# Performance work log

Hardware: AMD Instinct MI355X
Metric: run time of the kernel (lower is better)

Reference implementation:

```python
import jax, jax.numpy as jnp
import numpy as np

N = 100000      # nodes
E = 1600000     # edges (avg degree 16)
NFEAT = 16
HID = 64
OUT = 4
K = 3           # TAGConv hops
L = 4           # number of TAGConv layers


def setup_inputs() -> dict:
    key = jax.random.key(0)
    ks = jax.random.split(key, 6)
    x = jax.random.normal(ks[0], (N, NFEAT), dtype=jnp.float32)
    edge_index = jax.random.randint(ks[1], (2, E), 0, N, dtype=jnp.int64)
    # TAGConv has one (bias-free) linear per hop k=0..K, plus a per-layer bias.
    W0 = jax.random.normal(ks[2], (K + 1, NFEAT, HID), dtype=jnp.float32) * 0.1
    b0 = jnp.zeros((HID,), dtype=jnp.float32)
    Wh = jax.random.normal(ks[3], (L - 1, K + 1, HID, HID), dtype=jnp.float32) * 0.1
    bh = jnp.zeros((L - 1, HID), dtype=jnp.float32)
    fcW = jax.random.normal(ks[4], (HID, OUT), dtype=jnp.float32) * 0.1
    fcb = jnp.zeros((OUT,), dtype=jnp.float32)
    return dict(x=x, edge_index=edge_index, W0=W0, b0=b0, Wh=Wh, bh=bh, fcW=fcW, fcb=fcb)


def _gcn_norm(src, dst, num_nodes):
    # symmetric GCN normalization, no self-loops (PyG TAGConv default)
    ones = jnp.ones(src.shape, dtype=jnp.float32)
    deg = jax.ops.segment_sum(ones, dst, num_segments=num_nodes)
    dinv = jnp.where(deg > 0, 1.0 / jnp.sqrt(jnp.maximum(deg, 1e-12)), 0.0)
    return dinv[src] * dinv[dst]  # [E]


def _tag_conv(x, src, dst, norm, W, b):
    # out = sum_{k=0..K} (A_norm^k x) W_k + b
    out = x @ W[0]
    h = x
    for k in range(1, W.shape[0]):
        h = jax.ops.segment_sum(norm[:, None] * h[src], dst, num_segments=x.shape[0])
        out = out + h @ W[k]
    return out + b


def reference(x, edge_index, W0, b0, Wh, bh, fcW, fcb):
    src, dst = edge_index[0], edge_index[1]
    norm = _gcn_norm(src, dst, x.shape[0])
    h = jax.nn.relu(_tag_conv(x, src, dst, norm, W0, b0))  # conv0 (+relu, dropout=identity)
    for l in range(Wh.shape[0] - 1):  # middle convs with relu
        h = jax.nn.relu(_tag_conv(h, src, dst, norm, Wh[l], bh[l]))
    h = _tag_conv(h, src, dst, norm, Wh[-1], bh[-1])  # last conv, no relu
    return h @ fcW + fcb  # [N, OUT]
```

## Files before the change

kernel.cpp:

```cpp
#include <hip/hip_runtime.h>
#include <hip/hip_fp16.h>

constexpr int Nn   = 100000;
constexpr int Ne   = 1600000;
constexpr int NF   = 16;
constexpr int HID  = 64;
constexpr int NOUT = 4;

constexpr int NBUK  = 391;
constexpr int CHUNK = 2048;
constexpr int NB1   = (Ne + CHUNK - 1) / CHUNK;
constexpr int NS    = NBUK * NB1;
constexpr int STASH = 6144;

union H8 { float4 f4; __half h[8]; };
union H4 { float2 f2; __half h[4]; };


__global__ __launch_bounds__(256) void bhist_kernel(const int* __restrict__ dst,
                                                    int* __restrict__ ghist) {
    __shared__ int h[NBUK];
    int t = threadIdx.x;
    int b = blockIdx.x;
    for (int i = t; i < NBUK; i += 256) h[i] = 0;
    __syncthreads();
    int e0 = b * CHUNK;
    int e1 = (e0 + CHUNK < Ne) ? e0 + CHUNK : Ne;
    for (int e = e0 + t; e < e1; e += 256) atomicAdd(&h[dst[e] >> 8], 1);
    __syncthreads();
    for (int i = t; i < NBUK; i += 256) ghist[i * NB1 + b] = h[i];
}

__global__ __launch_bounds__(256) void scan1g_kernel(int* __restrict__ g,
                                                     int* __restrict__ bsum) {
    __shared__ int lds[256];
    int t = threadIdx.x;
    int base = blockIdx.x * 1024 + t * 4;
    int v0 = (base + 0 < NS) ? g[base + 0] : 0;
    int v1 = (base + 1 < NS) ? g[base + 1] : 0;
    int v2 = (base + 2 < NS) ? g[base + 2] : 0;
    int v3 = (base + 3 < NS) ? g[base + 3] : 0;
    lds[t] = v0 + v1 + v2 + v3;
    __syncthreads();
    for (int off = 1; off < 256; off <<= 1) {
        int a = lds[t];
        int b = (t >= off) ? lds[t - off] : 0;
        __syncthreads();
        lds[t] = a + b;
        __syncthreads();
    }
    int excl = (t > 0) ? lds[t - 1] : 0;
    if (base + 0 < NS) g[base + 0] = excl;
    if (base + 1 < NS) g[base + 1] = excl + v0;
    if (base + 2 < NS) g[base + 2] = excl + v0 + v1;
    if (base + 3 < NS) g[base + 3] = excl + v0 + v1 + v2;
    if (t == 255) bsum[blockIdx.x] = lds[255];
}

__global__ __launch_bounds__(512) void scan2g_kernel(int* __restrict__ bsum, int nb) {
    __shared__ int lds[512];
    int t = threadIdx.x;
    int v = (t < nb) ? bsum[t] : 0;
    lds[t] = v;
    __syncthreads();
    for (int off = 1; off < 512; off <<= 1) {
        int a = lds[t];
        int b = (t >= off) ? lds[t - off] : 0;
        __syncthreads();
        lds[t] = a + b;
        __syncthreads();
    }
    if (t < nb) bsum[t] = lds[t] - v;
}

__global__ __launch_bounds__(256) void scan3g_kernel(int* __restrict__ g,
                                                     const int* __restrict__ bsum) {
    int i = blockIdx.x * 256 + threadIdx.x;
    if (i < NS) g[i] += bsum[i >> 10];
}

__global__ __launch_bounds__(256) void bscatter_kernel(const int* __restrict__ src,
                                                       const int* __restrict__ dst,
                                                       const int* __restrict__ ghist,
                                                       int2* __restrict__ tmp) {
    __shared__ int hb[NBUK];
    __shared__ int cur[NBUK];
    int t = threadIdx.x;
    int b = blockIdx.x;
    for (int i = t; i < NBUK; i += 256) {
        hb[i] = ghist[i * NB1 + b];
        cur[i] = 0;
    }
    __syncthreads();
    int e0 = b * CHUNK;
    int e1 = (e0 + CHUNK < Ne) ? e0 + CHUNK : Ne;
    for (int e = e0 + t; e < e1; e += 256) {
        int d = dst[e];
        int s = src[e];
        int bin = d >> 8;
        int r = atomicAdd(&cur[bin], 1);
        tmp[hb[bin] + r] = make_int2(s, d);
    }
}

__global__ __launch_bounds__(256) void bcsr_kernel(const int2* __restrict__ tmp,
                                                   const int* __restrict__ ghist,
                                                   int* __restrict__ rowptr,
                                                   float* __restrict__ dinv,
                                                   int* __restrict__ colsrc) {
    __shared__ int2 stash[STASH];
    __shared__ int h[256];
    __shared__ int hs[256];
    __shared__ int cur[256];
    int t = threadIdx.x;
    int b = blockIdx.x;
    int lo = ghist[b * NB1];
    int hi = (b < NBUK - 1) ? ghist[(b + 1) * NB1] : Ne;
    int sz = hi - lo;
    h[t] = 0;
    cur[t] = 0;
    __syncthreads();
    for (int i = t; i < sz; i += 256) {
        int2 rec = tmp[lo + i];
        if (i < STASH) stash[i] = rec;
        atomicAdd(&h[rec.y & 255], 1);
    }
    __syncthreads();
    int myh = h[t];
    hs[t] = myh;
    __syncthreads();
    for (int off = 1; off < 256; off <<= 1) {
        int a = hs[t];
        int bb = (t >= off) ? hs[t - off] : 0;
        __syncthreads();
        hs[t] = a + bb;
        __syncthreads();
    }
    int excl = hs[t] - myh;
    __syncthreads();
    hs[t] = excl;
    int d = (b << 8) + t;
    if (d < Nn) {
        rowptr[d] = lo + excl;
        dinv[d] = (myh > 0) ? rsqrtf((float)myh) : 0.0f;
    }
    if (b == NBUK - 1 && t == 0) rowptr[Nn] = Ne;
    __syncthreads();
    for (int i = t; i < sz; i += 256) {
        int2 rec = (i < STASH) ? stash[i] : tmp[lo + i];
        int bin = rec.y & 255;
        int r = atomicAdd(&cur[bin], 1);
        colsrc[lo + hs[bin] + r] = rec.x;
    }
}

__global__ __launch_bounds__(256) void fill_kernel(const int* __restrict__ colsrc,
                                                   const float* __restrict__ dinv,
                                                   int2* __restrict__ edge2) {
    int e = blockIdx.x * 256 + threadIdx.x;
    if (e < Ne) {
        int s = colsrc[e];
        edge2[e] = make_int2(s, __float_as_int(dinv[s]));
    }
}

__global__ __launch_bounds__(256) void xcvt_kernel(const float* __restrict__ x,
                                                   __half* __restrict__ xh) {
    int i = blockIdx.x * 256 + threadIdx.x;
    if (i < Nn * NF / 4) {
        float4 v = reinterpret_cast<const float4*>(x)[i];
        H4 o;
        o.h[0] = __float2half(v.x);
        o.h[1] = __float2half(v.y);
        o.h[2] = __float2half(v.z);
        o.h[3] = __float2half(v.w);
        reinterpret_cast<float2*>(xh)[i] = o.f2;
    }
}


__global__ __launch_bounds__(256) void pull64h_kernel(const __half* __restrict__ hin,
                                                      const int* __restrict__ rowptr,
                                                      const int2* __restrict__ edge2,
                                                      const float* __restrict__ dinv,
                                                      __half* __restrict__ hout) {
    int lane = threadIdx.x & 63;
    int q  = lane & 3;
    int eo = (lane >> 2) & 3;
    int g  = lane >> 4;
    int n = blockIdx.x * 16 + (threadIdx.x >> 6) * 4 + g;
    if (n >= Nn) return;
    int r0 = rowptr[n];
    int r1 = rowptr[n + 1];
    float a[16];
#pragma unroll
    for (int j = 0; j < 16; ++j) a[j] = 0.f;
#pragma unroll 2
    for (int e = r0 + eo; e < r1; e += 4) {
        int2 ed = edge2[e];
        float w = __int_as_float(ed.y);
        const float4* rp = reinterpret_cast<const float4*>(hin + (size_t)ed.x * 64 + q * 16);
        H8 u0, u1;
        u0.f4 = rp[0];
        u1.f4 = rp[1];
#pragma unroll
        for (int j = 0; j < 8; ++j) a[j] += w * __half2float(u0.h[j]);
#pragma unroll
        for (int j = 0; j < 8; ++j) a[8 + j] += w * __half2float(u1.h[j]);
    }
#pragma unroll
    for (int off = 4; off <= 8; off <<= 1)
#pragma unroll
        for (int j = 0; j < 16; ++j) a[j] += __shfl_xor(a[j], off);
    if (eo == 0) {
        float dn = dinv[n];
        H8 o0, o1;
#pragma unroll
        for (int j = 0; j < 8; ++j) o0.h[j] = __float2half(a[j] * dn);
#pragma unroll
        for (int j = 0; j < 8; ++j) o1.h[j] = __float2half(a[8 + j] * dn);
        float4* op = reinterpret_cast<float4*>(hout + (size_t)n * 64 + q * 16);
        op[0] = o0.f4;
        op[1] = o1.f4;
    }
}

__global__ __launch_bounds__(256) void pull16h_kernel(const __half* __restrict__ hin,
                                                      const int* __restrict__ rowptr,
                                                      const int2* __restrict__ edge2,
                                                      const float* __restrict__ dinv,
                                                      __half* __restrict__ hout) {
    int lane = threadIdx.x & 63;
    int q  = lane & 1;
    int eo = (lane >> 1) & 3;
    int g  = lane >> 3;
    int n = blockIdx.x * 32 + (threadIdx.x >> 6) * 8 + g;
    if (n >= Nn) return;
    int r0 = rowptr[n];
    int r1 = rowptr[n + 1];
    float a[8];
#pragma unroll
    for (int j = 0; j < 8; ++j) a[j] = 0.f;
#pragma unroll 2
    for (int e = r0 + eo; e < r1; e += 4) {
        int2 ed = edge2[e];
        float w = __int_as_float(ed.y);
        H8 u;
        u.f4 = *reinterpret_cast<const float4*>(hin + (size_t)ed.x * 16 + q * 8);
#pragma unroll
        for (int j = 0; j < 8; ++j) a[j] += w * __half2float(u.h[j]);
    }
#pragma unroll
    for (int off = 2; off <= 4; off <<= 1)
#pragma unroll
        for (int j = 0; j < 8; ++j) a[j] += __shfl_xor(a[j], off);
    if (eo == 0) {
        float dn = dinv[n];
        H8 o;
#pragma unroll
        for (int j = 0; j < 8; ++j) o.h[j] = __float2half(a[j] * dn);
        *reinterpret_cast<float4*>(hout + (size_t)n * 16 + q * 8) = o.f4;
    }
}

template <int ADDBIAS>
__global__ __launch_bounds__(256) void pull4_kernel(const float* __restrict__ uin,
                                                    const float* __restrict__ gadd,
                                                    const int* __restrict__ rowptr,
                                                    const int2* __restrict__ edge2,
                                                    const float* __restrict__ dinv,
                                                    const float* __restrict__ beff,
                                                    float* __restrict__ out) {
    int lane = threadIdx.x & 63;
    int eo = lane & 15;
    int n = blockIdx.x * 16 + ((threadIdx.x >> 6) << 2) + (lane >> 4);
    if (n >= Nn) return;
    int r0 = rowptr[n];
    int r1 = rowptr[n + 1];
    float ax = 0.f, ay = 0.f, az = 0.f, aw = 0.f;
    for (int e = r0 + eo; e < r1; e += 16) {
        int2 ed = edge2[e];
        float w = __int_as_float(ed.y);
        float4 v = *reinterpret_cast<const float4*>(uin + (size_t)ed.x * 4);
        ax += w * v.x;
        ay += w * v.y;
        az += w * v.z;
        aw += w * v.w;
    }
#pragma unroll
    for (int off = 1; off < 16; off <<= 1) {
        ax += __shfl_xor(ax, off);
        ay += __shfl_xor(ay, off);
        az += __shfl_xor(az, off);
        aw += __shfl_xor(aw, off);
    }
    if (eo == 0) {
        float dn = dinv[n];
        float4 g = *reinterpret_cast<const float4*>(gadd + (size_t)n * 4);
        float4 o;
        o.x = g.x + dn * ax;
        o.y = g.y + dn * ay;
        o.z = g.z + dn * az;
        o.w = g.w + dn * aw;
        if (ADDBIAS) {
            o.x += beff[0]; o.y += beff[1]; o.z += beff[2]; o.w += beff[3];
        }
        *reinterpret_cast<float4*>(out + (size_t)n * 4) = o;
    }
}


template <int KS>
__global__ __launch_bounds__(256) void gemm4_kernel(const __half* __restrict__ S0,
                                                    const __half* __restrict__ S1,
                                                    const __half* __restrict__ S2,
                                                    const __half* __restrict__ S3,
                                                    const float* __restrict__ W,
                                                    const float* __restrict__ bias,
                                                    __half* __restrict__ out) {
    constexpr int PITCH = KS + 4;
    __shared__ float Ht[128 * PITCH];
    __shared__ float Wt[KS * 64];
    int t = threadIdx.x;
    int c4 = t & 15;
    int r8 = t >> 4;
    int r0 = blockIdx.x * 128;
    float acc[8][4];
#pragma unroll
    for (int j = 0; j < 8; ++j)
#pragma unroll
        for (int d = 0; d < 4; ++d) acc[j][d] = 0.f;

    const __half* Ss[4] = {S0, S1, S2, S3};
#pragma unroll
    for (int k = 0; k < 4; ++k) {
        const __half* S = Ss[k];
        for (int i = t; i < KS * 16; i += 256)
            *reinterpret_cast<float4*>(&Wt[i * 4]) =
                *reinterpret_cast<const float4*>(W + (size_t)k * KS * 64 + i * 4);
        for (int i = t; i < 128 * (KS / 8); i += 256) {
            int r = i / (KS / 8);
            int c8 = i % (KS / 8);
            int row = r0 + r;
            float* hp = &Ht[r * PITCH + c8 * 8];
            if (row < Nn) {
                H8 u;
                u.f4 = *reinterpret_cast<const float4*>(S + (size_t)row * KS + c8 * 8);
#pragma unroll
                for (int j = 0; j < 8; ++j) hp[j] = __half2float(u.h[j]);
            } else {
#pragma unroll
                for (int j = 0; j < 8; ++j) hp[j] = 0.f;
            }
        }
        __syncthreads();
#pragma unroll 4
        for (int f = 0; f < KS; ++f) {
            float4 b4 = *reinterpret_cast<const float4*>(&Wt[f * 64 + c4 * 4]);
#pragma unroll
            for (int j = 0; j < 8; ++j) {
                float a = Ht[(r8 + 16 * j) * PITCH + f];
                acc[j][0] += a * b4.x;
                acc[j][1] += a * b4.y;
                acc[j][2] += a * b4.z;
                acc[j][3] += a * b4.w;
            }
        }
        __syncthreads();
    }
    float4 bi = *reinterpret_cast<const float4*>(bias + c4 * 4);
#pragma unroll
    for (int j = 0; j < 8; ++j) {
        int row = r0 + r8 + 16 * j;
        if (row < Nn) {
            H4 o;
            o.h[0] = __float2half(fmaxf(acc[j][0] + bi.x, 0.f));
            o.h[1] = __float2half(fmaxf(acc[j][1] + bi.y, 0.f));
            o.h[2] = __float2half(fmaxf(acc[j][2] + bi.z, 0.f));
            o.h[3] = __float2half(fmaxf(acc[j][3] + bi.w, 0.f));
            *reinterpret_cast<float2*>(out + (size_t)row * 64 + c4 * 4) = o.f2;
        }
    }
}

__global__ __launch_bounds__(256) void weff_kernel(const float* __restrict__ W,
                                                   const float* __restrict__ b,
                                                   const float* __restrict__ fcW,
                                                   const float* __restrict__ fcb,
                                                   float* __restrict__ Wg,
                                                   float* __restrict__ beff) {
    int t = threadIdx.x;
    int k = t >> 6, c = t & 63;
    const float* wrow = W + (size_t)t * 64;
    float a0 = 0.f, a1 = 0.f, a2 = 0.f, a3 = 0.f;
    for (int d = 0; d < 64; ++d) {
        float w = wrow[d];
        a0 += w * fcW[d * 4 + 0];
        a1 += w * fcW[d * 4 + 1];
        a2 += w * fcW[d * 4 + 2];
        a3 += w * fcW[d * 4 + 3];
    }
    float4 o; o.x = a0; o.y = a1; o.z = a2; o.w = a3;
    *reinterpret_cast<float4*>(Wg + k * 256 + c * 4) = o;
    if (t < 4) {
        float s = fcb[t];
        for (int d = 0; d < 64; ++d) s += b[d] * fcW[d * 4 + t];
        beff[t] = s;
    }
}

__global__ __launch_bounds__(256) void gemmG_kernel(const __half* __restrict__ h,
                                                    const float* __restrict__ Wg,
                                                    float* __restrict__ G) {
    __shared__ float Ht[64 * 65];
    __shared__ float Wl[1024];
    int t = threadIdx.x;
    int r0 = blockIdx.x * 64;
    for (int i = t; i < 256; i += 256)
        *reinterpret_cast<float4*>(&Wl[i * 4]) = *reinterpret_cast<const float4*>(Wg + i * 4);
    for (int i = t; i < 64 * 8; i += 256) {
        int r = i >> 3;
        int c8 = i & 7;
        int row = r0 + r;
        float* hp = &Ht[r * 65 + c8 * 8];
        if (row < Nn) {
            H8 u;
            u.f4 = *reinterpret_cast<const float4*>(h + (size_t)row * 64 + c8 * 8);
#pragma unroll
            for (int j = 0; j < 8; ++j) hp[j] = __half2float(u.h[j]);
        } else {
#pragma unroll
            for (int j = 0; j < 8; ++j) hp[j] = 0.f;
        }
    }
    __syncthreads();
    int r = t & 63;
    int k = t >> 6;
    float a0 = 0.f, a1 = 0.f, a2 = 0.f, a3 = 0.f;
#pragma unroll 8
    for (int c = 0; c < 64; ++c) {
        float hv = Ht[r * 65 + c];
        const float* wp = &Wl[k * 256 + c * 4];
        a0 += hv * wp[0];
        a1 += hv * wp[1];
        a2 += hv * wp[2];
        a3 += hv * wp[3];
    }
    int row = r0 + r;
    if (row < Nn) {
        float4 o; o.x = a0; o.y = a1; o.z = a2; o.w = a3;
        *reinterpret_cast<float4*>(G + (size_t)k * Nn * 4 + (size_t)row * 4) = o;
    }
}


extern "C" void kernel_launch(void* const* d_in, const int* in_sizes, int n_in,
                              void* d_out, int out_size, void* d_ws, size_t ws_size,
                              hipStream_t stream) {
    const float* x   = (const float*)d_in[0];
    const int*   ei  = (const int*)d_in[1];
    const float* W0  = (const float*)d_in[2];
    const float* b0  = (const float*)d_in[3];
    const float* Wh  = (const float*)d_in[4];
    const float* bh  = (const float*)d_in[5];
    const float* fcW = (const float*)d_in[6];
    const float* fcb = (const float*)d_in[7];
    float* out = (float*)d_out;

    const int* src = ei;
    const int* dst = ei + Ne;

    int*    rowptr = (int*)d_ws;
    int2*   edge2  = (int2*)(rowptr + 100004);
    int*    ghist  = (int*)(rowptr + 100004 + 2 * Ne);
    int*    bsum   = ghist + 305792;
    float*  dinv   = (float*)(bsum + 512);
    float*  Wg     = dinv + Nn;
    float*  beff   = Wg + 1024;
    __half* xh     = (__half*)(beff + 16);
    __half* H0     = xh + (size_t)Nn * NF;
    __half* H1     = H0 + (size_t)Nn * HID;
    __half* H2     = H1 + (size_t)Nn * HID;
    __half* H3     = H2 + (size_t)Nn * HID;
    float*  G      = (float*)(H3 + (size_t)Nn * HID);
    float*  G0     = G + 0 * (size_t)Nn * 4;
    float*  G1     = G + 1 * (size_t)Nn * 4;
    float*  G2     = G + 2 * (size_t)Nn * 4;
    float*  G3     = G + 3 * (size_t)Nn * 4;
    float*  T      = G + 4 * (size_t)Nn * 4;
    float*  T2     = G + 5 * (size_t)Nn * 4;
    int2*   tmp    = (int2*)H2;
    int*    colsrc = (int*)H1;

    const int egrid  = (Ne + 255) / 256;
    const int s1grid = (NS + 1023) / 1024;
    const int s3grid = (NS + 255) / 256;
    const int p64grid = (Nn + 15) / 16;
    const int p16grid = (Nn + 31) / 32;
    const int ggrid  = (Nn + 127) / 128;
    const int qgrid  = (Nn + 15) / 16;
    const int Ggrid  = (Nn + 63) / 64;
    const int cgrid  = (Nn * NF / 4 + 255) / 256;

    bhist_kernel<<<NB1, 256, 0, stream>>>(dst, ghist);
    scan1g_kernel<<<s1grid, 256, 0, stream>>>(ghist, bsum);
    scan2g_kernel<<<1, 512, 0, stream>>>(bsum, s1grid);
    scan3g_kernel<<<s3grid, 256, 0, stream>>>(ghist, bsum);
    bscatter_kernel<<<NB1, 256, 0, stream>>>(src, dst, ghist, tmp);
    bcsr_kernel<<<NBUK, 256, 0, stream>>>(tmp, ghist, rowptr, dinv, colsrc);
    fill_kernel<<<egrid, 256, 0, stream>>>(colsrc, dinv, edge2);
    weff_kernel<<<1, 256, 0, stream>>>(Wh + 2 * 4 * 64 * 64, bh + 2 * 64, fcW, fcb, Wg, beff);
    xcvt_kernel<<<cgrid, 256, 0, stream>>>(x, xh);

    pull16h_kernel<<<p16grid, 256, 0, stream>>>(xh, rowptr, edge2, dinv, H1);
    pull16h_kernel<<<p16grid, 256, 0, stream>>>(H1, rowptr, edge2, dinv, H2);
    pull16h_kernel<<<p16grid, 256, 0, stream>>>(H2, rowptr, edge2, dinv, H3);
    gemm4_kernel<NF><<<ggrid, 256, 0, stream>>>(xh, H1, H2, H3, W0, b0, H0);

    for (int l = 0; l < 2; ++l) {
        pull64h_kernel<<<p64grid, 256, 0, stream>>>(H0, rowptr, edge2, dinv, H1);
        pull64h_kernel<<<p64grid, 256, 0, stream>>>(H1, rowptr, edge2, dinv, H2);
        pull64h_kernel<<<p64grid, 256, 0, stream>>>(H2, rowptr, edge2, dinv, H3);
        gemm4_kernel<HID><<<ggrid, 256, 0, stream>>>(H0, H1, H2, H3,
                                                     Wh + (size_t)l * 4 * HID * HID,
                                                     bh + (size_t)l * HID, H0);
    }

    gemmG_kernel<<<Ggrid, 256, 0, stream>>>(H0, Wg, G);
    pull4_kernel<0><<<qgrid, 256, 0, stream>>>(G3, G2, rowptr, edge2, dinv, beff, T);
    pull4_kernel<0><<<qgrid, 256, 0, stream>>>(T,  G1, rowptr, edge2, dinv, beff, T2);
    pull4_kernel<1><<<qgrid, 256, 0, stream>>>(T2, G0, rowptr, edge2, dinv, beff, out);
}
```

Baseline: 592.1 us.

## Replace scalar fp32 hop GEMMs with MFMA f16 matrix-core kernels

Replaces the shared-memory fp32 FMA GEMM that combines the four hop features with a wave-level kernel using 16x16x32 f16 MFMA instructions. Operands are read straight from global memory with no LDS staging. Weights are pre-packed once per call into an fp16 fragment layout by a new small kernel. This cuts ALU work and shared-memory traffic in the GEMMs, at the cost of fp16 weights, scalar half-precision output stores and three extra tiny launches.

```diff
diff --git a/kernel.cpp b/kernel.cpp
--- a/kernel.cpp
+++ b/kernel.cpp
@@ -15,6 +15,9 @@
 
 union H8 { float4 f4; __half h[8]; };
 union H4 { float2 f2; __half h[4]; };
+
+typedef _Float16 f16x8 __attribute__((ext_vector_type(8)));
+typedef float    f32x4 __attribute__((ext_vector_type(4)));
 
 
 __global__ __launch_bounds__(256) void bhist_kernel(const int* __restrict__ dst,
@@ -309,76 +312,77 @@
     }
 }
 
-
 template <int KS>
-__global__ __launch_bounds__(256) void gemm4_kernel(const __half* __restrict__ S0,
-                                                    const __half* __restrict__ S1,
-                                                    const __half* __restrict__ S2,
-                                                    const __half* __restrict__ S3,
-                                                    const float* __restrict__ W,
-                                                    const float* __restrict__ bias,
-                                                    __half* __restrict__ out) {
-    constexpr int PITCH = KS + 4;
-    __shared__ float Ht[128 * PITCH];
-    __shared__ float Wt[KS * 64];
-    int t = threadIdx.x;
-    int c4 = t & 15;
-    int r8 = t >> 4;
-    int r0 = blockIdx.x * 128;
-    float acc[8][4];
-#pragma unroll
-    for (int j = 0; j < 8; ++j)
-#pragma unroll
-        for (int d = 0; d < 4; ++d) acc[j][d] = 0.f;
-
+__global__ __launch_bounds__(256) void wfrag_kernel(const float* __restrict__ W,
+                                                    __half* __restrict__ Wfrag) {
+    constexpr int NT = (4 * KS / 32) * 4 * 64;
+    int tid = blockIdx.x * 256 + threadIdx.x;
+    if (tid >= NT) return;
+    int l  = tid & 63;
+    int ct = (tid >> 6) & 3;
+    int ks = tid >> 8;
+    int c  = ct * 16 + (l & 15);
+    int kb = ks * 32 + (l >> 4) * 8;
+    H8 o;
+#pragma unroll
+    for (int j = 0; j < 8; ++j) {
+        int k = kb + j;
+        o.h[j] = __float2half(W[(size_t)(k / KS) * KS * 64 + (size_t)(k % KS) * 64 + c]);
+    }
+    *reinterpret_cast<float4*>(Wfrag + (size_t)tid * 8) = o.f4;
+}
+
+
+template <int KS, int RELU>
+__global__ __launch_bounds__(256) void gemm4m_kernel(const __half* __restrict__ S0,
+                                                     const __half* __restrict__ S1,
+                                                     const __half* __restrict__ S2,
+                                                     const __half* __restrict__ S3,
+                                                     const __half* __restrict__ Wfrag,
+                                                     const float* __restrict__ bias,
+                                                     __half* __restrict__ out) {
+    constexpr int NKS = 4 * KS / 32;
+    int lane = threadIdx.x & 63;
+    int wv = threadIdx.x >> 6;
+    int base = blockIdx.x * 128 + wv * 32;
+    int r = lane & 15;
+    int qa = lane >> 4;
+    int acol = qa * 8;
     const __half* Ss[4] = {S0, S1, S2, S3};
-#pragma unroll
-    for (int k = 0; k < 4; ++k) {
-        const __half* S = Ss[k];
-        for (int i = t; i < KS * 16; i += 256)
-            *reinterpret_cast<float4*>(&Wt[i * 4]) =
-                *reinterpret_cast<const float4*>(W + (size_t)k * KS * 64 + i * 4);
-        for (int i = t; i < 128 * (KS / 8); i += 256) {
-            int r = i / (KS / 8);
-            int c8 = i % (KS / 8);
-            int row = r0 + r;
-            float* hp = &Ht[r * PITCH + c8 * 8];
-            if (row < Nn) {
-                H8 u;
-                u.f4 = *reinterpret_cast<const float4*>(S + (size_t)row * KS + c8 * 8);
-#pragma unroll
-                for (int j = 0; j < 8; ++j) hp[j] = __half2float(u.h[j]);
-            } else {
-#pragma unroll
-                for (int j = 0; j < 8; ++j) hp[j] = 0.f;
+    f32x4 acc[2][4] = {};
+    int row0 = base + r;       if (row0 >= Nn) row0 = Nn - 1;
+    int row1 = base + 16 + r;  if (row1 >= Nn) row1 = Nn - 1;
+#pragma unroll
+    for (int ks = 0; ks < NKS; ++ks) {
+        int k0 = ks * 32 + acol;
+        const __half* Sa = Ss[k0 / KS];
+        int col = k0 % KS;
+        f16x8 a0 = *reinterpret_cast<const f16x8*>(Sa + (size_t)row0 * KS + col);
+        f16x8 a1 = *reinterpret_cast<const f16x8*>(Sa + (size_t)row1 * KS + col);
+        const __half* wp = Wfrag + ((size_t)(ks * 4) * 64 + lane) * 8;
+#pragma unroll
+        for (int ct = 0; ct < 4; ++ct) {
+            f16x8 b = *reinterpret_cast<const f16x8*>(wp + (size_t)ct * 64 * 8);
+            acc[0][ct] = __builtin_amdgcn_mfma_f32_16x16x32_f16(a0, b, acc[0][ct], 0, 0, 0);
+            acc[1][ct] = __builtin_amdgcn_mfma_f32_16x16x32_f16(a1, b, acc[1][ct], 0, 0, 0);
+        }
+    }
+    int ccol = lane & 15;
+    int rb = (lane >> 4) * 4;
+#pragma unroll
+    for (int rt = 0; rt < 2; ++rt) {
+#pragma unroll
+        for (int ct = 0; ct < 4; ++ct) {
+            float bi = bias[ct * 16 + ccol];
+#pragma unroll
+            for (int i = 0; i < 4; ++i) {
+                int row = base + rt * 16 + rb + i;
+                if (row < Nn) {
+                    float v = acc[rt][ct][i] + bi;
+                    if (RELU) v = fmaxf(v, 0.f);
+                    out[(size_t)row * 64 + ct * 16 + ccol] = __float2half(v);
+                }
             }
-        }
-        __syncthreads();
-#pragma unroll 4
-        for (int f = 0; f < KS; ++f) {
-            float4 b4 = *reinterpret_cast<const float4*>(&Wt[f * 64 + c4 * 4]);
-#pragma unroll
-            for (int j = 0; j < 8; ++j) {
-                float a = Ht[(r8 + 16 * j) * PITCH + f];
-                acc[j][0] += a * b4.x;
-                acc[j][1] += a * b4.y;
-                acc[j][2] += a * b4.z;
-                acc[j][3] += a * b4.w;
-            }
-        }
-        __syncthreads();
-    }
-    float4 bi = *reinterpret_cast<const float4*>(bias + c4 * 4);
-#pragma unroll
-    for (int j = 0; j < 8; ++j) {
-        int row = r0 + r8 + 16 * j;
-        if (row < Nn) {
-            H4 o;
-            o.h[0] = __float2half(fmaxf(acc[j][0] + bi.x, 0.f));
-            o.h[1] = __float2half(fmaxf(acc[j][1] + bi.y, 0.f));
-            o.h[2] = __float2half(fmaxf(acc[j][2] + bi.z, 0.f));
-            o.h[3] = __float2half(fmaxf(acc[j][3] + bi.w, 0.f));
-            *reinterpret_cast<float2*>(out + (size_t)row * 64 + c4 * 4) = o.f2;
         }
     }
 }
@@ -477,7 +481,10 @@
     float*  dinv   = (float*)(bsum + 512);
     float*  Wg     = dinv + Nn;
     float*  beff   = Wg + 1024;
-    __half* xh     = (__half*)(beff + 16);
+    __half* Wf0    = (__half*)(beff + 16);
+    __half* Wf1    = Wf0 + 4096;
+    __half* Wf2    = Wf1 + 16384;
+    __half* xh     = Wf2 + 16384;
     __half* H0     = xh + (size_t)Nn * NF;
     __half* H1     = H0 + (size_t)Nn * HID;
     __half* H2     = H1 + (size_t)Nn * HID;
@@ -511,19 +518,22 @@
     fill_kernel<<<egrid, 256, 0, stream>>>(colsrc, dinv, edge2);
     weff_kernel<<<1, 256, 0, stream>>>(Wh + 2 * 4 * 64 * 64, bh + 2 * 64, fcW, fcb, Wg, beff);
     xcvt_kernel<<<cgrid, 256, 0, stream>>>(x, xh);
+    wfrag_kernel<16><<<2, 256, 0, stream>>>(W0, Wf0);
+    wfrag_kernel<64><<<8, 256, 0, stream>>>(Wh + 0 * 4 * 64 * 64, Wf1);
+    wfrag_kernel<64><<<8, 256, 0, stream>>>(Wh + 1 * 4 * 64 * 64, Wf2);
 
     pull16h_kernel<<<p16grid, 256, 0, stream>>>(xh, rowptr, edge2, dinv, H1);
     pull16h_kernel<<<p16grid, 256, 0, stream>>>(H1, rowptr, edge2, dinv, H2);
     pull16h_kernel<<<p16grid, 256, 0, stream>>>(H2, rowptr, edge2, dinv, H3);
-    gemm4_kernel<NF><<<ggrid, 256, 0, stream>>>(xh, H1, H2, H3, W0, b0, H0);
+    gemm4m_kernel<16, 1><<<ggrid, 256, 0, stream>>>(xh, H1, H2, H3, Wf0, b0, H0);
 
     for (int l = 0; l < 2; ++l) {
         pull64h_kernel<<<p64grid, 256, 0, stream>>>(H0, rowptr, edge2, dinv, H1);
         pull64h_kernel<<<p64grid, 256, 0, stream>>>(H1, rowptr, edge2, dinv, H2);
         pull64h_kernel<<<p64grid, 256, 0, stream>>>(H2, rowptr, edge2, dinv, H3);
-        gemm4_kernel<HID><<<ggrid, 256, 0, stream>>>(H0, H1, H2, H3,
-                                                     Wh + (size_t)l * 4 * HID * HID,
-                                                     bh + (size_t)l * HID, H0);
+        gemm4m_kernel<64, 1><<<ggrid, 256, 0, stream>>>(H0, H1, H2, H3,
+                                                        (l == 0) ? Wf1 : Wf2,
+                                                        bh + (size_t)l * HID, H0);
     }
 
     gemmG_kernel<<<Ggrid, 256, 0, stream>>>(H0, Wg, G);
```

After: 510.3 us. -13.8%, faster.
